# Kernel tuning notes

Hardware: AMD Instinct MI355X
Metric: run time of the kernel (lower is better)

The kernel has to match this reference:

```python
import jax, jax.numpy as jnp
import numpy as np

B, L, C, D = 4, 128, 1024, 512

def setup_inputs() -> dict:
    key = jax.random.key(0)
    ks = jax.random.split(key, 6)
    scale = 1.0 / np.sqrt(D)
    return {
        "hidden": jax.random.normal(ks[0], (B, L, D), dtype=jnp.float32),
        "ctx": jax.random.normal(ks[1], (B, C, D), dtype=jnp.float32),
        "W": jax.random.normal(ks[2], (D, D), dtype=jnp.float32) * scale,
        "U": jax.random.normal(ks[3], (D, D), dtype=jnp.float32) * scale,
        "U_b": jax.random.normal(ks[4], (D,), dtype=jnp.float32) * scale,
        "V": jax.random.normal(ks[5], (D,), dtype=jnp.float32) * scale,
    }

def reference(hidden, ctx, W, U, U_b, V):
    # Bahdanau additive attention: softmax_j V . tanh(W h_i + U c_j + b)
    wq = jnp.einsum('bld,ed->ble', hidden, W)          # [B, L, D]
    uc = jnp.einsum('bcd,ed->bce', ctx, U) + U_b       # [B, C, D]
    s = jnp.tanh(wq[:, :, None, :] + uc[:, None, :, :])  # [B, L, C, D]
    align = jnp.einsum('blcd,d->blc', s, V)            # [B, L, C]
    return jax.nn.softmax(align, axis=-1)
```

## Files before the change

kernel.cpp:

```cpp
#include <hip/hip_runtime.h>
#include <hip/hip_bf16.h>


#define SCALE2 2.8853900817779268f

typedef _Float16 f16x8 __attribute__((ext_vector_type(8)));
typedef float f32x4 __attribute__((ext_vector_type(4)));

__device__ __forceinline__ void gload16(const void* g, void* l) {
    __builtin_amdgcn_global_load_lds(
        (const __attribute__((address_space(1))) void*)g,
        (__attribute__((address_space(3))) void*)l,
        16, 0, 0);
}

__global__ __launch_bounds__(256) void gemm_mfma(
    const float* __restrict__ hidden, const float* __restrict__ ctx,
    const float* __restrict__ Wmat, const float* __restrict__ Umat,
    const float* __restrict__ U_b,
    float* __restrict__ ewq_t, float* __restrict__ euc_t)
{
    __shared__ __align__(16) _Float16 Xh[2][64][40];
    __shared__ __align__(16) _Float16 Xl[2][64][40];
    __shared__ __align__(16) _Float16 Wh[2][64][40];
    __shared__ __align__(16) _Float16 Wl[2][64][40];

    const int tid  = threadIdx.x;
    const int lane = tid & 63;
    const int w    = tid >> 6;

    const float *X, *Wm, *bias;
    float* Ct;
    int m0, crow0, Mb, bshift;
    {
        int gb = blockIdx.x;
        if (gb < 64) {
            m0 = (gb & 7) * 64; crow0 = (gb >> 3) * 64;
            X = hidden; Wm = Wmat; bias = nullptr; Ct = ewq_t; Mb = 128; bshift = 7;
        } else {
            int g = gb - 64;
            m0 = (g & 7) * 64; crow0 = (g >> 3) * 64;
            X = ctx; Wm = Umat; bias = U_b; Ct = euc_t; Mb = 1024; bshift = 10;
        }
    }

    const int sr = tid >> 2;
    const int sk = (tid & 3) * 8;
    const float* xsrc = X  + (size_t)(crow0 + sr) * 512 + sk;
    const float* wsrc = Wm + (size_t)(m0    + sr) * 512 + sk;

    f32x4 acc[4];
#pragma unroll
    for (int t = 0; t < 4; ++t) acc[t] = (f32x4){0.f, 0.f, 0.f, 0.f};

    float xr[8], wr[8];
    {
        float4 a = *(const float4*)(xsrc);
        float4 b = *(const float4*)(xsrc + 4);
        float4 c = *(const float4*)(wsrc);
        float4 d = *(const float4*)(wsrc + 4);
        xr[0]=a.x; xr[1]=a.y; xr[2]=a.z; xr[3]=a.w; xr[4]=b.x; xr[5]=b.y; xr[6]=b.z; xr[7]=b.w;
        wr[0]=c.x; wr[1]=c.y; wr[2]=c.z; wr[3]=c.w; wr[4]=d.x; wr[5]=d.y; wr[6]=d.z; wr[7]=d.w;
        f16x8 xh, xl, wh, wl;
#pragma unroll
        for (int i = 0; i < 8; ++i) {
            xh[i] = (_Float16)xr[i]; xl[i] = (_Float16)(xr[i] - (float)xh[i]);
            wh[i] = (_Float16)wr[i]; wl[i] = (_Float16)(wr[i] - (float)wh[i]);
        }
        *(f16x8*)&Xh[0][sr][sk] = xh; *(f16x8*)&Xl[0][sr][sk] = xl;
        *(f16x8*)&Wh[0][sr][sk] = wh; *(f16x8*)&Wl[0][sr][sk] = wl;
    }

    const int fr = lane & 15;
    const int fk = (lane >> 4) * 8;
    const int mrow = w * 16 + fr;

    for (int kc = 0; kc < 16; ++kc) {
        if (kc < 15) {
            float4 a = *(const float4*)(xsrc + (kc + 1) * 32);
            float4 b = *(const float4*)(xsrc + (kc + 1) * 32 + 4);
            float4 c = *(const float4*)(wsrc + (kc + 1) * 32);
            float4 d = *(const float4*)(wsrc + (kc + 1) * 32 + 4);
            xr[0]=a.x; xr[1]=a.y; xr[2]=a.z; xr[3]=a.w; xr[4]=b.x; xr[5]=b.y; xr[6]=b.z; xr[7]=b.w;
            wr[0]=c.x; wr[1]=c.y; wr[2]=c.z; wr[3]=c.w; wr[4]=d.x; wr[5]=d.y; wr[6]=d.z; wr[7]=d.w;
        }
        __syncthreads();
        const int bu = kc & 1;
        const f16x8 ah = *(const f16x8*)&Wh[bu][mrow][fk];
        const f16x8 al = *(const f16x8*)&Wl[bu][mrow][fk];
#pragma unroll
        for (int t = 0; t < 4; ++t) {
            const f16x8 bh = *(const f16x8*)&Xh[bu][t * 16 + fr][fk];
            const f16x8 bl = *(const f16x8*)&Xl[bu][t * 16 + fr][fk];
            acc[t] = __builtin_amdgcn_mfma_f32_16x16x32_f16(ah, bh, acc[t], 0, 0, 0);
            acc[t] = __builtin_amdgcn_mfma_f32_16x16x32_f16(ah, bl, acc[t], 0, 0, 0);
            acc[t] = __builtin_amdgcn_mfma_f32_16x16x32_f16(al, bh, acc[t], 0, 0, 0);
        }
        if (kc < 15) {
            f16x8 xh, xl, wh, wl;
#pragma unroll
            for (int i = 0; i < 8; ++i) {
                xh[i] = (_Float16)xr[i]; xl[i] = (_Float16)(xr[i] - (float)xh[i]);
                wh[i] = (_Float16)wr[i]; wl[i] = (_Float16)(wr[i] - (float)wh[i]);
            }
            *(f16x8*)&Xh[bu ^ 1][sr][sk] = xh; *(f16x8*)&Xl[bu ^ 1][sr][sk] = xl;
            *(f16x8*)&Wh[bu ^ 1][sr][sk] = wh; *(f16x8*)&Wl[bu ^ 1][sr][sk] = wl;
        }
    }

    const int rbase = m0 + w * 16 + (lane >> 4) * 4;
    float bl4[4] = {0.f, 0.f, 0.f, 0.f};
    if (bias) {
        float4 t = *(const float4*)&bias[rbase];
        bl4[0] = t.x; bl4[1] = t.y; bl4[2] = t.z; bl4[3] = t.w;
    }
    const int bidx = crow0 >> bshift;
    const int cl0  = crow0 & (Mb - 1);
    float* obase = Ct + ((size_t)bidx * 512 + rbase) * Mb + cl0 + fr;
#pragma unroll
    for (int r = 0; r < 4; ++r)
#pragma unroll
        for (int t = 0; t < 4; ++t)
            obase[(size_t)r * Mb + t * 16] =
                __builtin_amdgcn_exp2f(SCALE2 * (acc[t][r] + bl4[r]));
}

__global__ __launch_bounds__(256) void fused_align7(
    const float* __restrict__ ewq_t,
    const float* __restrict__ euc_t,
    const float* __restrict__ Vv,
    float* __restrict__ p0, float* __restrict__ p1,
    float* __restrict__ p2, float* __restrict__ p3)
{
    __shared__ __align__(16) float uc_s[2][32][256];
    __shared__ __align__(16) float wq_s[2][32][16];
    __shared__ float v_s[128];

    const int tid  = threadIdx.x;
    const int lane = tid & 63;
    const int w    = __builtin_amdgcn_readfirstlane(tid >> 6);
    const int c0   = blockIdx.x * 256;
    const int l0   = blockIdx.y * 16;
    const int z    = blockIdx.z;
    const int b    = z >> 2, h = z & 3;
    const int d0   = h * 128;

    const float* ucb = euc_t + ((size_t)b * 512 + d0) * 1024 + c0;
    const float* wqb = ewq_t + ((size_t)b * 512 + d0) * 128 + l0;

    if (tid < 128) v_s[tid] = Vv[d0 + tid];

#define STAGE(buf, chunk)                                                     \
    {                                                                         \
        const float* src_ = ucb + (size_t)((chunk) * 32) * 1024;              \
        _Pragma("unroll")                                                     \
        for (int i_ = 0; i_ < 8; ++i_) {                                      \
            const int d_ = w * 8 + i_;                                        \
            gload16(src_ + (size_t)d_ * 1024 + lane * 4, &uc_s[buf][d_][0]);  \
        }                                                                     \
        if (w < 2) {                                                          \
            const float* ws_ = wqb + (size_t)((chunk) * 32 + w * 16) * 128;   \
            gload16(ws_ + (size_t)(lane >> 2) * 128 + (lane & 3) * 4,         \
                    &wq_s[buf][w * 16][0]);                                   \
        }                                                                     \
    }

    float4 acc[4];
#pragma unroll
    for (int i = 0; i < 4; ++i) acc[i] = make_float4(0.f, 0.f, 0.f, 0.f);

    STAGE(0, 0);
    __syncthreads();

    for (int k = 0; k < 4; ++k) {
        if (k < 3) STAGE((k + 1) & 1, k + 1);
        const int bu = k & 1;
#pragma unroll 4
        for (int d = 0; d < 32; ++d) {
            const float4 e = *(const float4*)&uc_s[bu][d][lane * 4];
            const float4 q = *(const float4*)&wq_s[bu][d][w * 4];
            const float vv = v_s[k * 32 + d];
            const float qc[4] = {q.x, q.y, q.z, q.w};
#pragma unroll
            for (int i = 0; i < 4; ++i) {
                acc[i].x = fmaf(vv, __builtin_amdgcn_rcpf(fmaf(qc[i], e.x, 1.0f)), acc[i].x);
                acc[i].y = fmaf(vv, __builtin_amdgcn_rcpf(fmaf(qc[i], e.y, 1.0f)), acc[i].y);
                acc[i].z = fmaf(vv, __builtin_amdgcn_rcpf(fmaf(qc[i], e.z, 1.0f)), acc[i].z);
                acc[i].w = fmaf(vv, __builtin_amdgcn_rcpf(fmaf(qc[i], e.w, 1.0f)), acc[i].w);
            }
        }
        __syncthreads();
    }
#undef STAGE

    float* pp = (h == 0) ? p0 : (h == 1) ? p1 : (h == 2) ? p2 : p3;
#pragma unroll
    for (int i = 0; i < 4; ++i) {
        float4 r;
        r.x = -2.0f * acc[i].x; r.y = -2.0f * acc[i].y;
        r.z = -2.0f * acc[i].z; r.w = -2.0f * acc[i].w;
        *(float4*)(pp + ((size_t)b * 128 + l0 + w * 4 + i) * 1024 + c0 + lane * 4) = r;
    }
}

__global__ __launch_bounds__(256) void softmax3(
    float* __restrict__ data, const float* __restrict__ p1,
    const float* __restrict__ p2, const float* __restrict__ p3)
{
    const int row  = blockIdx.x * 4 + (threadIdx.x >> 6);
    const int lane = threadIdx.x & 63;
    float* p = data + (size_t)row * 1024;
    const float* q1 = p1 + (size_t)row * 1024;
    const float* q2 = p2 + (size_t)row * 1024;
    const float* q3 = p3 + (size_t)row * 1024;

    float4 x[4];
#pragma unroll
    for (int j = 0; j < 4; ++j) {
        float4 a = *(const float4*)(p  + j * 256 + lane * 4);
        float4 b = *(const float4*)(q1 + j * 256 + lane * 4);
        float4 c = *(const float4*)(q2 + j * 256 + lane * 4);
        float4 d = *(const float4*)(q3 + j * 256 + lane * 4);
        x[j].x = (a.x + b.x) + (c.x + d.x);
        x[j].y = (a.y + b.y) + (c.y + d.y);
        x[j].z = (a.z + b.z) + (c.z + d.z);
        x[j].w = (a.w + b.w) + (c.w + d.w);
    }

    float m = x[0].x;
#pragma unroll
    for (int j = 0; j < 4; ++j) {
        m = fmaxf(m, x[j].x); m = fmaxf(m, x[j].y);
        m = fmaxf(m, x[j].z); m = fmaxf(m, x[j].w);
    }
#pragma unroll
    for (int mask = 32; mask >= 1; mask >>= 1) m = fmaxf(m, __shfl_xor(m, mask, 64));

    const float LOG2E = 1.4426950408889634f;
    float s = 0.0f;
#pragma unroll
    for (int j = 0; j < 4; ++j) {
        x[j].x = __builtin_amdgcn_exp2f((x[j].x - m) * LOG2E);
        x[j].y = __builtin_amdgcn_exp2f((x[j].y - m) * LOG2E);
        x[j].z = __builtin_amdgcn_exp2f((x[j].z - m) * LOG2E);
        x[j].w = __builtin_amdgcn_exp2f((x[j].w - m) * LOG2E);
        s += x[j].x + x[j].y + x[j].z + x[j].w;
    }
#pragma unroll
    for (int mask = 32; mask >= 1; mask >>= 1) s += __shfl_xor(s, mask, 64);
    const float r = __builtin_amdgcn_rcpf(s);
#pragma unroll
    for (int j = 0; j < 4; ++j) {
        x[j].x *= r; x[j].y *= r; x[j].z *= r; x[j].w *= r;
        *(float4*)(p + j * 256 + lane * 4) = x[j];
    }
}

extern "C" void kernel_launch(void* const* d_in, const int* in_sizes, int n_in,
                              void* d_out, int out_size, void* d_ws, size_t ws_size,
                              hipStream_t stream)
{
    const float* hidden = (const float*)d_in[0];
    const float* ctx    = (const float*)d_in[1];
    const float* W      = (const float*)d_in[2];
    const float* U      = (const float*)d_in[3];
    const float* U_b    = (const float*)d_in[4];
    const float* V      = (const float*)d_in[5];
    float* out = (float*)d_out;

    float* ewq_t = (float*)d_ws;
    float* euc_t = ewq_t + 4 * 512 * 128;
    float* p1    = euc_t + 4 * 512 * 1024;
    float* p2    = p1 + 4 * 128 * 1024;
    float* p3    = p2 + 4 * 128 * 1024;

    gemm_mfma<<<576, 256, 0, stream>>>(hidden, ctx, W, U, U_b, ewq_t, euc_t);
    fused_align7<<<dim3(4, 8, 16), 256, 0, stream>>>(ewq_t, euc_t, V, out, p1, p2, p3);
    softmax3<<<128, 256, 0, stream>>>(out, p1, p2, p3);
}
```

Baseline: 59.41 us.

## Pair reciprocals across d and retile align kernel to smaller column tiles

```diff
diff --git a/kernel.cpp b/kernel.cpp
--- a/kernel.cpp
+++ b/kernel.cpp
@@ -125,81 +125,111 @@
                 __builtin_amdgcn_exp2f(SCALE2 * (acc[t][r] + bl4[r]));
 }
 
-__global__ __launch_bounds__(256) void fused_align7(
+__global__ __launch_bounds__(256) void fused_align8(
     const float* __restrict__ ewq_t,
     const float* __restrict__ euc_t,
     const float* __restrict__ Vv,
     float* __restrict__ p0, float* __restrict__ p1,
     float* __restrict__ p2, float* __restrict__ p3)
 {
-    __shared__ __align__(16) float uc_s[2][32][256];
-    __shared__ __align__(16) float wq_s[2][32][16];
-    __shared__ float v_s[128];
+    __shared__ __align__(16) float uc_s[2][16][128];
+    __shared__ float2 v2_s[64];
 
     const int tid  = threadIdx.x;
     const int lane = tid & 63;
     const int w    = __builtin_amdgcn_readfirstlane(tid >> 6);
-    const int c0   = blockIdx.x * 256;
+    const int c0   = blockIdx.x * 128;
     const int l0   = blockIdx.y * 16;
     const int z    = blockIdx.z;
     const int b    = z >> 2, h = z & 3;
     const int d0   = h * 128;
 
     const float* ucb = euc_t + ((size_t)b * 512 + d0) * 1024 + c0;
-    const float* wqb = ewq_t + ((size_t)b * 512 + d0) * 128 + l0;
-
-    if (tid < 128) v_s[tid] = Vv[d0 + tid];
+    const float* wqb = ewq_t + ((size_t)b * 512 + d0) * 128 + l0 + w * 4;
+
+    if (tid < 64)
+        v2_s[tid] = make_float2(Vv[d0 + 2 * tid], Vv[d0 + 2 * tid + 1]);
 
 #define STAGE(buf, chunk)                                                     \
     {                                                                         \
-        const float* src_ = ucb + (size_t)((chunk) * 32) * 1024;              \
+        const float* s_ = ucb +                                               \
+            (size_t)((chunk) * 16 + w * 4 + (lane >> 5)) * 1024 +             \
+            (lane & 31) * 4;                                                  \
+        gload16(s_,        &uc_s[buf][w * 4][0]);                             \
+        gload16(s_ + 2048, &uc_s[buf][w * 4 + 2][0]);                         \
+    }
+
+#define QLOAD(Q, chunk)                                                       \
+    {                                                                         \
         _Pragma("unroll")                                                     \
-        for (int i_ = 0; i_ < 8; ++i_) {                                      \
-            const int d_ = w * 8 + i_;                                        \
-            gload16(src_ + (size_t)d_ * 1024 + lane * 4, &uc_s[buf][d_][0]);  \
+        for (int j_ = 0; j_ < 16; ++j_)                                       \
+            Q[j_] = *(const float4*)(wqb + (size_t)((chunk) * 16 + j_) * 128);\
+    }
+
+    float acc[4][2];
+#pragma unroll
+    for (int i = 0; i < 4; ++i) { acc[i][0] = 0.f; acc[i][1] = 0.f; }
+
+#define COMPUTE(buf, Q, ch)                                                   \
+    {                                                                         \
+        _Pragma("unroll")                                                     \
+        for (int j = 0; j < 8; ++j) {                                         \
+            const float2 e0 = *(const float2*)&uc_s[buf][2 * j][lane * 2];    \
+            const float2 e1 = *(const float2*)&uc_s[buf][2 * j + 1][lane * 2];\
+            const float2 vp = v2_s[(ch) * 8 + j];                             \
+            const float4 q0 = Q[2 * j], q1 = Q[2 * j + 1];                    \
+            const float q0a[4] = {q0.x, q0.y, q0.z, q0.w};                    \
+            const float q1a[4] = {q1.x, q1.y, q1.z, q1.w};                    \
+            const float e0a[2] = {e0.x, e0.y};                                \
+            const float e1a[2] = {e1.x, e1.y};                                \
+            _Pragma("unroll")                                                 \
+            for (int i = 0; i < 4; ++i) {                                     \
+                _Pragma("unroll")                                             \
+                for (int k = 0; k < 2; ++k) {                                 \
+                    const float t0 = fmaf(q0a[i], e0a[k], 1.0f);              \
+                    const float t1 = fmaf(q1a[i], e1a[k], 1.0f);              \
+                    const float den = t0 * t1;                                \
+                    const float n = fmaf(vp.x, t1, vp.y * t0);                \
+                    acc[i][k] = fmaf(n, __builtin_amdgcn_rcpf(den), acc[i][k]);\
+                }                                                             \
+            }                                                                 \
         }                                                                     \
-        if (w < 2) {                                                          \
-            const float* ws_ = wqb + (size_t)((chunk) * 32 + w * 16) * 128;   \
-            gload16(ws_ + (size_t)(lane >> 2) * 128 + (lane & 3) * 4,         \
-                    &wq_s[buf][w * 16][0]);                                   \
-        }                                                                     \
-    }
-
-    float4 acc[4];
-#pragma unroll
-    for (int i = 0; i < 4; ++i) acc[i] = make_float4(0.f, 0.f, 0.f, 0.f);
-
+    }
+
+    float4 qa[16], qb[16];
     STAGE(0, 0);
+    QLOAD(qa, 0);
     __syncthreads();
 
-    for (int k = 0; k < 4; ++k) {
-        if (k < 3) STAGE((k + 1) & 1, k + 1);
-        const int bu = k & 1;
-#pragma unroll 4
-        for (int d = 0; d < 32; ++d) {
-            const float4 e = *(const float4*)&uc_s[bu][d][lane * 4];
-            const float4 q = *(const float4*)&wq_s[bu][d][w * 4];
-            const float vv = v_s[k * 32 + d];
-            const float qc[4] = {q.x, q.y, q.z, q.w};
-#pragma unroll
-            for (int i = 0; i < 4; ++i) {
-                acc[i].x = fmaf(vv, __builtin_amdgcn_rcpf(fmaf(qc[i], e.x, 1.0f)), acc[i].x);
-                acc[i].y = fmaf(vv, __builtin_amdgcn_rcpf(fmaf(qc[i], e.y, 1.0f)), acc[i].y);
-                acc[i].z = fmaf(vv, __builtin_amdgcn_rcpf(fmaf(qc[i], e.z, 1.0f)), acc[i].z);
-                acc[i].w = fmaf(vv, __builtin_amdgcn_rcpf(fmaf(qc[i], e.w, 1.0f)), acc[i].w);
+#pragma unroll
+    for (int cc = 0; cc < 4; ++cc) {
+        const int ch0 = cc * 2, ch1 = cc * 2 + 1;
+        {
+            STAGE(1, ch0 + 1);
+            QLOAD(qb, ch0 + 1);
+            COMPUTE(0, qa, ch0);
+            __syncthreads();
+        }
+        {
+            if (ch1 < 7) {
+                STAGE(0, ch1 + 1);
+                QLOAD(qa, ch1 + 1);
             }
-        }
-        __syncthreads();
+            COMPUTE(1, qb, ch1);
+            __syncthreads();
+        }
     }
 #undef STAGE
+#undef QLOAD
+#undef COMPUTE
 
     float* pp = (h == 0) ? p0 : (h == 1) ? p1 : (h == 2) ? p2 : p3;
 #pragma unroll
     for (int i = 0; i < 4; ++i) {
-        float4 r;
-        r.x = -2.0f * acc[i].x; r.y = -2.0f * acc[i].y;
-        r.z = -2.0f * acc[i].z; r.w = -2.0f * acc[i].w;
-        *(float4*)(pp + ((size_t)b * 128 + l0 + w * 4 + i) * 1024 + c0 + lane * 4) = r;
+        float2 r;
+        r.x = -2.0f * acc[i][0];
+        r.y = -2.0f * acc[i][1];
+        *(float2*)(pp + ((size_t)b * 128 + l0 + w * 4 + i) * 1024 + c0 + lane * 2) = r;
     }
 }
 
@@ -275,6 +305,6 @@
     float* p3    = p2 + 4 * 128 * 1024;
 
     gemm_mfma<<<576, 256, 0, stream>>>(hidden, ctx, W, U, U_b, ewq_t, euc_t);
-    fused_align7<<<dim3(4, 8, 16), 256, 0, stream>>>(ewq_t, euc_t, V, out, p1, p2, p3);
+    fused_align8<<<dim3(8, 8, 16), 256, 0, stream>>>(ewq_t, euc_t, V, out, p1, p2, p3);
     softmax3<<<128, 256, 0, stream>>>(out, p1, p2, p3);
 }
```

After: 181.2 us. 3.05x slower.
